# Kernel tuning notes

Hardware: AMD Instinct MI355X
Metric: run time of the kernel (lower is better)

Reference implementation:

```python
import jax, jax.numpy as jnp
import numpy as np

DIM = 512        # model dim
MOE_DIM = 256    # expert hidden dim
E = 64           # n_routed experts
G = 8            # n_routed_group
TOPK_G = 4       # n_topk_group
K = 8            # n_experts_per_tok
SCALE = 2.5      # routed_scale
CAP = 1024


def setup_inputs() -> dict:
    key = jax.random.key(0)
    ks = jax.random.split(key, 6)
    x = jax.random.normal(ks[0], (4, 512, DIM), jnp.float32)
    gate_w = jax.random.normal(ks[1], (E, DIM), jnp.float32) / np.sqrt(DIM).astype(np.float32)
    gate_b = jax.random.normal(ks[2], (E,), jnp.float32) * 0.01
    w1 = jax.random.normal(ks[3], (E, DIM, MOE_DIM), jnp.float32) / np.sqrt(DIM).astype(np.float32)
    w3 = jax.random.normal(ks[4], (E, DIM, MOE_DIM), jnp.float32) / np.sqrt(DIM).astype(np.float32)
    w2 = jax.random.normal(ks[5], (E, MOE_DIM, DIM), jnp.float32) / np.sqrt(MOE_DIM).astype(np.float32)
    return {"x": x, "gate_w": gate_w, "gate_b": gate_b, "w1": w1, "w3": w3, "w2": w2}


def _gate(x2, gate_w, gate_b):
    # x2: [T, DIM] -> (weights [T,K], indices [T,K])
    T = x2.shape[0]
    scores = jax.nn.sigmoid(x2 @ gate_w.T)                      # [T, E]
    s = (scores + gate_b).reshape(T, G, E // G)                  # grouped scores
    group_scores = jax.lax.top_k(s, 2)[0].sum(-1)                # [T, G] sum of top-2 per group
    top_groups = jax.lax.top_k(group_scores, TOPK_G)[1]          # [T, TOPK_G]
    gmask = jnp.zeros((T, G), bool).at[jnp.arange(T)[:, None], top_groups].set(True)
    s = jnp.where(gmask[..., None], s, -jnp.inf).reshape(T, E)
    idx = jax.lax.top_k(s, K)[1]                                 # [T, K]
    w = jnp.take_along_axis(scores, idx, axis=1)                 # original (pre-bias) scores
    w = w / w.sum(-1, keepdims=True) * SCALE
    return w, idx


def _moe_forward(x, gate_w, gate_b, w1, w3, w2):
    shape = x.shape
    x2 = x.reshape(-1, DIM)                                      # [T, DIM]
    T = x2.shape[0]
    w, idx = _gate(x2, gate_w, gate_b)
    flat_e = idx.reshape(-1)                                     # [T*K]
    # position of each (token, slot) within its expert's buffer, in order
    oh = (flat_e[:, None] == jnp.arange(E)[None, :]).astype(jnp.int32)  # [T*K, E]
    pos = (jnp.cumsum(oh, axis=0) * oh).sum(-1) - 1              # [T*K]
    x_rep = jnp.repeat(x2, K, axis=0)                            # [T*K, DIM]
    # dispatch into per-expert buffers [E, CAP, DIM]
    xb = jnp.zeros((E, CAP, DIM), x2.dtype).at[flat_e, pos].set(x_rep, mode='drop')
    h = jax.nn.silu(jnp.einsum('ecd,edm->ecm', xb, w1)) * jnp.einsum('ecd,edm->ecm', xb, w3)
    yb = jnp.einsum('ecm,emd->ecd', h, w2)                       # [E, CAP, DIM]
    # combine: gather back and weight
    y = yb.at[flat_e, pos].get(mode='fill', fill_value=0.0) * w.reshape(-1)[:, None]
    return y.reshape(T, K, DIM).sum(1).reshape(shape)


def reference(x, gate_w, gate_b, w1, w3, w2):
    return _moe_forward(x, gate_w, gate_b, w1, w3, w2)
```

## Files before the change

kernel.cpp:

```cpp
#include <hip/hip_runtime.h>

#define T_TOK 2048
#define DIM   512
#define MOE   256
#define NE    64
#define NG    8
#define TOPKG 4
#define TOPK  8
#define CAP   1024
#define MOE_SCALE 2.5f

typedef float f32x4 __attribute__((ext_vector_type(4)));
typedef short s16x8 __attribute__((ext_vector_type(8)));

__device__ __forceinline__ unsigned short f2bf(float f) {
    unsigned u = __builtin_bit_cast(unsigned, f);
    unsigned r = (u + 0x7fffu + ((u >> 16) & 1u)) >> 16;
    return (unsigned short)r;
}
__device__ __forceinline__ unsigned pk2(float lo, float hi) {
    return (unsigned)f2bf(lo) | ((unsigned)f2bf(hi) << 16);
}

__device__ __forceinline__ void tile_scan(const int* __restrict__ counts, int lane,
                                          int e, int& G0, int& ne, int& nt)
{
    int cl = min(counts[lane], CAP);
    int ntl = (cl + 31) >> 5;
    int v = ntl;
#pragma unroll
    for (int d = 1; d < 64; d <<= 1) {
        int o = __shfl_up(v, d);
        if (lane >= d) v += o;
    }
    G0 = __shfl(v - ntl, e);
    ne = __shfl(cl, e);
    nt = __shfl(ntl, e);
}

__global__ __launch_bounds__(256) void gwt_k(const float* __restrict__ gw,
                                             float* __restrict__ gwT)
{
    int idx = blockIdx.x * 256 + threadIdx.x;
    int e = idx >> 9, k = idx & 511;
    gwT[(size_t)(k >> 2) * 256 + e * 4 + (k & 3)] = gw[idx];
}

__global__ __launch_bounds__(256) void gate_fused_k(const float* __restrict__ x,
                                                    const float* __restrict__ gwT,
                                                    const float* __restrict__ gb,
                                                    int* __restrict__ counts,
                                                    int* __restrict__ etok,
                                                    float* __restrict__ wt_of,
                                                    short* __restrict__ xb)
{
    __shared__ float xs[4][512];
    __shared__ float ps[4][4][64];
    int w = threadIdx.x >> 6, lane = threadIdx.x & 63;
    int t = blockIdx.x * 4 + w;

    {
        const float4* xr = (const float4*)(x + (size_t)t * DIM);
        float4 v0 = xr[lane * 2], v1 = xr[lane * 2 + 1];
        *(float4*)&xs[w][lane * 8]     = v0;
        *(float4*)&xs[w][lane * 8 + 4] = v1;
        short o[8];
        o[0] = (short)f2bf(v0.x); o[1] = (short)f2bf(v0.y);
        o[2] = (short)f2bf(v0.z); o[3] = (short)f2bf(v0.w);
        o[4] = (short)f2bf(v1.x); o[5] = (short)f2bf(v1.y);
        o[6] = (short)f2bf(v1.z); o[7] = (short)f2bf(v1.w);
        *(s16x8*)(xb + (size_t)t * DIM + lane * 8) = *(const s16x8*)o;
    }
    __syncthreads();

    const f32x4* gt = (const f32x4*)gwT;
    float a0 = 0.f, a1 = 0.f, a2 = 0.f, a3 = 0.f;
    int kb = w * 32;
#pragma unroll 8
    for (int k4 = 0; k4 < 32; ++k4) {
        f32x4 g  = gt[(size_t)(kb + k4) * 64 + lane];
        f32x4 x0 = *(const f32x4*)&xs[0][(kb + k4) * 4];
        f32x4 x1 = *(const f32x4*)&xs[1][(kb + k4) * 4];
        f32x4 x2 = *(const f32x4*)&xs[2][(kb + k4) * 4];
        f32x4 x3 = *(const f32x4*)&xs[3][(kb + k4) * 4];
        a0 += g.x * x0.x + g.y * x0.y + g.z * x0.z + g.w * x0.w;
        a1 += g.x * x1.x + g.y * x1.y + g.z * x1.z + g.w * x1.w;
        a2 += g.x * x2.x + g.y * x2.y + g.z * x2.z + g.w * x2.w;
        a3 += g.x * x3.x + g.y * x3.y + g.z * x3.z + g.w * x3.w;
    }
    ps[w][0][lane] = a0; ps[w][1][lane] = a1;
    ps[w][2][lane] = a2; ps[w][3][lane] = a3;
    __syncthreads();
    float acc = ps[0][w][lane] + ps[1][w][lane] + ps[2][w][lane] + ps[3][w][lane];

    float sc = 1.f / (1.f + __expf(-acc));
    float s  = sc + gb[lane];

    float m1 = s, m2 = -1e30f;
#pragma unroll
    for (int d = 1; d < 8; d <<= 1) {
        float o1 = __shfl_xor(m1, d);
        float o2 = __shfl_xor(m2, d);
        float n1 = fmaxf(m1, o1);
        float n2 = fmaxf(fminf(m1, o1), fmaxf(m2, o2));
        m1 = n1; m2 = n2;
    }
    float gv = m1 + m2;

    bool gkeep = false;
#pragma unroll
    for (int it = 0; it < TOPKG; ++it) {
        float m = gv;
#pragma unroll
        for (int d = 1; d < 64; d <<= 1) m = fmaxf(m, __shfl_xor(m, d));
        unsigned long long mask = __ballot(gv == m);
        int ldr = __ffsll(mask) - 1;
        if ((lane >> 3) == (ldr >> 3)) { gkeep = true; gv = -2e30f; }
    }
    float sv = gkeep ? s : -1e30f;

    float wsum = 0.f;
    int my_e = 0; float my_w = 0.f;
#pragma unroll
    for (int k = 0; k < TOPK; ++k) {
        float m = sv;
#pragma unroll
        for (int d = 1; d < 64; d <<= 1) m = fmaxf(m, __shfl_xor(m, d));
        unsigned long long mask = __ballot(sv == m);
        int l = __ffsll(mask) - 1;
        float wk = __shfl(sc, l);
        wsum += wk;
        if (lane == k) { my_e = l; my_w = wk; }
        if (lane == l) sv = -2e30f;
    }
    float scale = MOE_SCALE / wsum;
    if (lane < TOPK) {
        int p = atomicAdd(&counts[my_e], 1);
        int rid = t * TOPK + lane;
        bool ok = (p < CAP);
        if (ok) etok[my_e * CAP + p] = rid;
        wt_of[rid] = ok ? my_w * scale : 0.f;
    }
}

__global__ __launch_bounds__(256, 2) void gemm1_k(const short* __restrict__ xb,
                                                  const float* __restrict__ w1,
                                                  const float* __restrict__ w3,
                                                  const int* __restrict__ counts,
                                                  const int* __restrict__ etok,
                                                  short* __restrict__ hgf)
{
    __shared__ short Bl[2][16][2][64][8];
    __shared__ short Ct[4][2][16][24];

    int e  = blockIdx.x & 63, cg = blockIdx.x >> 6;
    int n0 = cg * 32;
    int tid = threadIdx.x;
    int w = tid >> 6, lane = tid & 63;
    int q = lane >> 4, m16 = lane & 15;

    int G0, ne, nt;
    tile_scan(counts, lane, e, G0, ne, nt);

    const float* W1e = w1 + (size_t)e * DIM * MOE + n0;
    const float* W3e = w3 + (size_t)e * DIM * MOE + n0;
#pragma unroll 4
    for (int it = 0; it < 16; ++it) {
        int idx = it * 256 + tid;
        int mat = idx >> 11;
        int rem = idx & 2047;
        int r2  = rem >> 3;
        int cq  = (rem & 7) * 4;
        int k   = r2 * 2;
        int kt = k >> 5, qf = (k >> 3) & 3, j0 = k & 7;
        int cgrp = cq >> 4, c15 = cq & 15;
        const float* p = (mat ? W3e : W1e) + (size_t)k * MOE + cq;
        f32x4 lo = *(const f32x4*)p;
        f32x4 hi = *(const f32x4*)(p + MOE);
        unsigned* b = (unsigned*)&Bl[mat][kt][cgrp][qf * 16 + c15][j0];
        b[0]  = pk2(lo.x, hi.x);
        b[4]  = pk2(lo.y, hi.y);
        b[8]  = pk2(lo.z, hi.z);
        b[12] = pk2(lo.w, hi.w);
    }
    __syncthreads();

    const int* el = etok + e * CAP;

    int row0 = w * 32 + m16, row1 = row0 + 16;
    int tr0 = 0, tr1 = 0;
    if (w < nt) {
        tr0 = el[row0 < ne ? row0 : ne - 1];
        tr1 = el[row1 < ne ? row1 : ne - 1];
    }

    for (int T = w; T < nt; T += 4) {
        const short* A0 = xb + (size_t)(tr0 >> 3) * DIM + q * 8;
        const short* A1 = xb + (size_t)(tr1 >> 3) * DIM + q * 8;
        if (T + 4 < nt) {
            int nr0 = (T + 4) * 32 + m16, nr1 = nr0 + 16;
            tr0 = el[nr0 < ne ? nr0 : ne - 1];
            tr1 = el[nr1 < ne ? nr1 : ne - 1];
        }

        f32x4 acc[2][2][2];
#pragma unroll
        for (int i = 0; i < 2; ++i)
#pragma unroll
            for (int j = 0; j < 2; ++j)
#pragma unroll
                for (int c = 0; c < 2; ++c) acc[i][j][c] = (f32x4)0.f;

        s16x8 pa0[8], pa1[8];
#pragma unroll
        for (int i = 0; i < 8; ++i) {
            pa0[i] = *(const s16x8*)(A0 + i * 32);
            pa1[i] = *(const s16x8*)(A1 + i * 32);
        }
#pragma unroll
        for (int kt = 0; kt < 16; ++kt) {
            s16x8 a0 = pa0[kt & 7], a1 = pa1[kt & 7];
            if (kt < 8) {
                pa0[kt & 7] = *(const s16x8*)(A0 + (kt + 8) * 32);
                pa1[kt & 7] = *(const s16x8*)(A1 + (kt + 8) * 32);
            }
            s16x8 b10 = *(const s16x8*)&Bl[0][kt][0][lane][0];
            s16x8 b11 = *(const s16x8*)&Bl[0][kt][1][lane][0];
            s16x8 b30 = *(const s16x8*)&Bl[1][kt][0][lane][0];
            s16x8 b31 = *(const s16x8*)&Bl[1][kt][1][lane][0];
            acc[0][0][0] = __builtin_amdgcn_mfma_f32_16x16x32_bf16(a0, b10, acc[0][0][0], 0, 0, 0);
            acc[1][0][0] = __builtin_amdgcn_mfma_f32_16x16x32_bf16(a1, b10, acc[1][0][0], 0, 0, 0);
            acc[0][0][1] = __builtin_amdgcn_mfma_f32_16x16x32_bf16(a0, b11, acc[0][0][1], 0, 0, 0);
            acc[1][0][1] = __builtin_amdgcn_mfma_f32_16x16x32_bf16(a1, b11, acc[1][0][1], 0, 0, 0);
            acc[0][1][0] = __builtin_amdgcn_mfma_f32_16x16x32_bf16(a0, b30, acc[0][1][0], 0, 0, 0);
            acc[1][1][0] = __builtin_amdgcn_mfma_f32_16x16x32_bf16(a1, b30, acc[1][1][0], 0, 0, 0);
            acc[0][1][1] = __builtin_amdgcn_mfma_f32_16x16x32_bf16(a0, b31, acc[0][1][1], 0, 0, 0);
            acc[1][1][1] = __builtin_amdgcn_mfma_f32_16x16x32_bf16(a1, b31, acc[1][1][1], 0, 0, 0);
        }

#pragma unroll
        for (int cgrp = 0; cgrp < 2; ++cgrp) {
#pragma unroll
            for (int sub = 0; sub < 2; ++sub)
#pragma unroll
                for (int r = 0; r < 4; ++r) {
                    float g = acc[sub][0][cgrp][r];
                    float u = acc[sub][1][cgrp][r];
                    float hv = g / (1.f + __expf(-g)) * u;
                    Ct[w][sub][q * 4 + r][m16] = (short)f2bf(hv);
                }
            int subr = q >> 1;
            s16x8 hv8 = *(const s16x8*)&Ct[w][subr][m16][(q & 1) * 8];
            size_t slot = ((size_t)(G0 + T) * 8 + cg) * 2 + subr;
            *(s16x8*)(hgf + slot * 512 + (cgrp * 2 + (q & 1)) * 128 + m16 * 8) = hv8;
        }
    }
}

__global__ __launch_bounds__(256, 2) void gemm2_k(const short* __restrict__ hgf,
                                                  const float* __restrict__ w2,
                                                  const int* __restrict__ counts,
                                                  const int* __restrict__ etok,
                                                  const float* __restrict__ wt_of,
                                                  float* __restrict__ out)
{
    __shared__ short Bl[4][8][64][8];

    int e  = blockIdx.x & 63, cg = blockIdx.x >> 6;
    int n0 = cg * 64;
    int tid = threadIdx.x;
    int w = tid >> 6, lane = tid & 63;
    int q = lane >> 4, m16 = lane & 15;

    int G0, ne, nt;
    tile_scan(counts, lane, e, G0, ne, nt);

    const float* W2e = w2 + (size_t)e * MOE * DIM + n0;
#pragma unroll 4
    for (int it = 0; it < 8; ++it) {
        int idx = it * 256 + tid;
        int r2  = idx >> 4;
        int cq  = (idx & 15) * 4;
        int k   = r2 * 2;
        int kt2 = k >> 5, qf = (k >> 3) & 3, j0 = k & 7;
        int s = cq >> 4, c15 = cq & 15;
        const float* p = W2e + (size_t)k * DIM + cq;
        f32x4 lo = *(const f32x4*)p;
        f32x4 hi = *(const f32x4*)(p + DIM);
        unsigned* b = (unsigned*)&Bl[s][kt2][qf * 16 + c15][j0];
        b[0]  = pk2(lo.x, hi.x);
        b[4]  = pk2(lo.y, hi.y);
        b[8]  = pk2(lo.z, hi.z);
        b[12] = pk2(lo.w, hi.w);
    }
    __syncthreads();

    const int* el = etok + e * CAP;

    for (int T = w; T < nt; T += 4) {
        const short* A = hgf + (size_t)(G0 + T) * 8192 + lane * 8;

        int   erid[2][4];
        float wtr[2][4];
#pragma unroll
        for (int sub = 0; sub < 2; ++sub)
#pragma unroll
            for (int r = 0; r < 4; ++r) {
                int row = T * 32 + sub * 16 + q * 4 + r;
                int rid = row < ne ? el[row] : -1;
                erid[sub][r] = rid;
                wtr[sub][r]  = rid >= 0 ? wt_of[rid] : 0.f;
            }

        s16x8 pa[16];
#pragma unroll
        for (int i = 0; i < 16; ++i)
            pa[i] = *(const s16x8*)(A + i * 512);

        f32x4 acc[2][4];
#pragma unroll
        for (int i = 0; i < 2; ++i)
#pragma unroll
            for (int j = 0; j < 4; ++j) acc[i][j] = (f32x4)0.f;

#pragma unroll
        for (int kt = 0; kt < 8; ++kt) {
            s16x8 a0 = pa[kt * 2], a1 = pa[kt * 2 + 1];
            s16x8 b0 = *(const s16x8*)&Bl[0][kt][lane][0];
            s16x8 b1 = *(const s16x8*)&Bl[1][kt][lane][0];
            s16x8 b2 = *(const s16x8*)&Bl[2][kt][lane][0];
            s16x8 b3 = *(const s16x8*)&Bl[3][kt][lane][0];
            acc[0][0] = __builtin_amdgcn_mfma_f32_16x16x32_bf16(a0, b0, acc[0][0], 0, 0, 0);
            acc[1][0] = __builtin_amdgcn_mfma_f32_16x16x32_bf16(a1, b0, acc[1][0], 0, 0, 0);
            acc[0][1] = __builtin_amdgcn_mfma_f32_16x16x32_bf16(a0, b1, acc[0][1], 0, 0, 0);
            acc[1][1] = __builtin_amdgcn_mfma_f32_16x16x32_bf16(a1, b1, acc[1][1], 0, 0, 0);
            acc[0][2] = __builtin_amdgcn_mfma_f32_16x16x32_bf16(a0, b2, acc[0][2], 0, 0, 0);
            acc[1][2] = __builtin_amdgcn_mfma_f32_16x16x32_bf16(a1, b2, acc[1][2], 0, 0, 0);
            acc[0][3] = __builtin_amdgcn_mfma_f32_16x16x32_bf16(a0, b3, acc[0][3], 0, 0, 0);
            acc[1][3] = __builtin_amdgcn_mfma_f32_16x16x32_bf16(a1, b3, acc[1][3], 0, 0, 0);
        }

#pragma unroll
        for (int sub = 0; sub < 2; ++sub)
#pragma unroll
            for (int r = 0; r < 4; ++r) {
                int rid = erid[sub][r];
                if (rid >= 0) {
                    float* op = out + (size_t)(rid >> 3) * DIM + n0 + m16;
                    float wk = wtr[sub][r];
#pragma unroll
                    for (int s = 0; s < 4; ++s)
                        atomicAdd(op + s * 16, wk * acc[sub][s][r]);
                }
            }
    }
}

extern "C" void kernel_launch(void* const* d_in, const int* in_sizes, int n_in,
                              void* d_out, int out_size, void* d_ws, size_t ws_size,
                              hipStream_t stream)
{
    const float* x  = (const float*)d_in[0];
    const float* gw = (const float*)d_in[1];
    const float* gb = (const float*)d_in[2];
    const float* w1 = (const float*)d_in[3];
    const float* w3 = (const float*)d_in[4];
    const float* w2 = (const float*)d_in[5];

    char* ws = (char*)d_ws;
    short* xb    = (short*)(ws);
    short* hgf   = (short*)(ws + 2097152);
    float* gwT   = (float*)(ws + 28311552);
    int*   etok  = (int*)  (ws + 28442624);
    float* wt_of = (float*)(ws + 28704768);
    int*   counts= (int*)  (ws + 28770304);

    hipMemsetAsync(counts, 0, NE * 4, stream);
    hipMemsetAsync(d_out, 0, (size_t)T_TOK * DIM * 4, stream);

    gwt_k<<<128, 256, 0, stream>>>(gw, gwT);
    gate_fused_k<<<T_TOK / 4, 256, 0, stream>>>(x, gwT, gb, counts, etok, wt_of, xb);
    gemm1_k<<<NE * 8, 256, 0, stream>>>(xb, w1, w3, counts, etok, hgf);
    gemm2_k<<<NE * 8, 256, 0, stream>>>(hgf, w2, counts, etok, wt_of, (float*)d_out);
}
```

Measured before the change: 270.1 us.

## Replace atomic scatter-add with bf16 per-slot buffer and combine kernel; double block size

gemm2 now writes each expert output row as bf16 into a per-(token,slot) buffer instead of doing fp32 atomicAdd into the output. A new combine kernel then sums the 8 weighted slots per token, which also removes the output memset. Both GEMM kernels move to 512-thread blocks with 8 waves sharing the staged weight tile, and the weight loads become nontemporal. The trade is an extra kernel launch, a round trip through a buffer, and bf16 rounding of the expert outputs before they are combined.

```diff
diff --git a/kernel.cpp b/kernel.cpp
--- a/kernel.cpp
+++ b/kernel.cpp
@@ -143,7 +143,7 @@
     }
 }
 
-__global__ __launch_bounds__(256, 2) void gemm1_k(const short* __restrict__ xb,
+__global__ __launch_bounds__(512, 4) void gemm1_k(const short* __restrict__ xb,
                                                   const float* __restrict__ w1,
                                                   const float* __restrict__ w3,
                                                   const int* __restrict__ counts,
@@ -151,7 +151,7 @@
                                                   short* __restrict__ hgf)
 {
     __shared__ short Bl[2][16][2][64][8];
-    __shared__ short Ct[4][2][16][24];
+    __shared__ short Ct[8][2][16][24];
 
     int e  = blockIdx.x & 63, cg = blockIdx.x >> 6;
     int n0 = cg * 32;
@@ -165,8 +165,8 @@
     const float* W1e = w1 + (size_t)e * DIM * MOE + n0;
     const float* W3e = w3 + (size_t)e * DIM * MOE + n0;
 #pragma unroll 4
-    for (int it = 0; it < 16; ++it) {
-        int idx = it * 256 + tid;
+    for (int it = 0; it < 8; ++it) {
+        int idx = it * 512 + tid;
         int mat = idx >> 11;
         int rem = idx & 2047;
         int r2  = rem >> 3;
@@ -175,8 +175,8 @@
         int kt = k >> 5, qf = (k >> 3) & 3, j0 = k & 7;
         int cgrp = cq >> 4, c15 = cq & 15;
         const float* p = (mat ? W3e : W1e) + (size_t)k * MOE + cq;
-        f32x4 lo = *(const f32x4*)p;
-        f32x4 hi = *(const f32x4*)(p + MOE);
+        f32x4 lo = __builtin_nontemporal_load((const f32x4*)p);
+        f32x4 hi = __builtin_nontemporal_load((const f32x4*)(p + MOE));
         unsigned* b = (unsigned*)&Bl[mat][kt][cgrp][qf * 16 + c15][j0];
         b[0]  = pk2(lo.x, hi.x);
         b[4]  = pk2(lo.y, hi.y);
@@ -194,11 +194,11 @@
         tr1 = el[row1 < ne ? row1 : ne - 1];
     }
 
-    for (int T = w; T < nt; T += 4) {
+    for (int T = w; T < nt; T += 8) {
         const short* A0 = xb + (size_t)(tr0 >> 3) * DIM + q * 8;
         const short* A1 = xb + (size_t)(tr1 >> 3) * DIM + q * 8;
-        if (T + 4 < nt) {
-            int nr0 = (T + 4) * 32 + m16, nr1 = nr0 + 16;
+        if (T + 8 < nt) {
+            int nr0 = (T + 8) * 32 + m16, nr1 = nr0 + 16;
             tr0 = el[nr0 < ne ? nr0 : ne - 1];
             tr1 = el[nr1 < ne ? nr1 : ne - 1];
         }
@@ -257,12 +257,11 @@
     }
 }
 
-__global__ __launch_bounds__(256, 2) void gemm2_k(const short* __restrict__ hgf,
+__global__ __launch_bounds__(512, 4) void gemm2_k(const short* __restrict__ hgf,
                                                   const float* __restrict__ w2,
                                                   const int* __restrict__ counts,
                                                   const int* __restrict__ etok,
-                                                  const float* __restrict__ wt_of,
-                                                  float* __restrict__ out)
+                                                  short* __restrict__ ybuf)
 {
     __shared__ short Bl[4][8][64][8];
 
@@ -277,16 +276,16 @@
 
     const float* W2e = w2 + (size_t)e * MOE * DIM + n0;
 #pragma unroll 4
-    for (int it = 0; it < 8; ++it) {
-        int idx = it * 256 + tid;
+    for (int it = 0; it < 4; ++it) {
+        int idx = it * 512 + tid;
         int r2  = idx >> 4;
         int cq  = (idx & 15) * 4;
         int k   = r2 * 2;
         int kt2 = k >> 5, qf = (k >> 3) & 3, j0 = k & 7;
         int s = cq >> 4, c15 = cq & 15;
         const float* p = W2e + (size_t)k * DIM + cq;
-        f32x4 lo = *(const f32x4*)p;
-        f32x4 hi = *(const f32x4*)(p + DIM);
+        f32x4 lo = __builtin_nontemporal_load((const f32x4*)p);
+        f32x4 hi = __builtin_nontemporal_load((const f32x4*)(p + DIM));
         unsigned* b = (unsigned*)&Bl[s][kt2][qf * 16 + c15][j0];
         b[0]  = pk2(lo.x, hi.x);
         b[4]  = pk2(lo.y, hi.y);
@@ -297,19 +296,16 @@
 
     const int* el = etok + e * CAP;
 
-    for (int T = w; T < nt; T += 4) {
+    for (int T = w; T < nt; T += 8) {
         const short* A = hgf + (size_t)(G0 + T) * 8192 + lane * 8;
 
-        int   erid[2][4];
-        float wtr[2][4];
+        int erid[2][4];
 #pragma unroll
         for (int sub = 0; sub < 2; ++sub)
 #pragma unroll
             for (int r = 0; r < 4; ++r) {
                 int row = T * 32 + sub * 16 + q * 4 + r;
-                int rid = row < ne ? el[row] : -1;
-                erid[sub][r] = rid;
-                wtr[sub][r]  = rid >= 0 ? wt_of[rid] : 0.f;
+                erid[sub][r] = row < ne ? el[row] : -1;
             }
 
         s16x8 pa[16];
@@ -343,17 +339,35 @@
 #pragma unroll
         for (int sub = 0; sub < 2; ++sub)
 #pragma unroll
-            for (int r = 0; r < 4; ++r) {
-                int rid = erid[sub][r];
-                if (rid >= 0) {
-                    float* op = out + (size_t)(rid >> 3) * DIM + n0 + m16;
-                    float wk = wtr[sub][r];
-#pragma unroll
-                    for (int s = 0; s < 4; ++s)
-                        atomicAdd(op + s * 16, wk * acc[sub][s][r]);
+            for (int s = 0; s < 4; ++s)
+#pragma unroll
+                for (int r = 0; r < 4; ++r) {
+                    if (erid[sub][r] >= 0)
+                        ybuf[(size_t)erid[sub][r] * DIM + n0 + s * 16 + m16] =
+                            (short)f2bf(acc[sub][s][r]);
                 }
-            }
-    }
+    }
+}
+
+__global__ __launch_bounds__(256) void combine_k(const short* __restrict__ ybuf,
+                                                 const float* __restrict__ wt_of,
+                                                 float* __restrict__ out)
+{
+    int t = blockIdx.x;
+    int tid = threadIdx.x;
+    const int* yb = (const int*)ybuf;
+    float sx = 0.f, sy = 0.f;
+#pragma unroll
+    for (int k = 0; k < TOPK; ++k) {
+        float wk = wt_of[t * TOPK + k];
+        int v = yb[(size_t)(t * TOPK + k) * (DIM / 2) + tid];
+        float lo = __builtin_bit_cast(float, (unsigned)v << 16);
+        float hi = __builtin_bit_cast(float, (unsigned)v & 0xffff0000u);
+        sx += wk * lo;
+        sy += wk * hi;
+    }
+    float2 o = {sx, sy};
+    ((float2*)out)[(size_t)t * (DIM / 2) + tid] = o;
 }
 
 extern "C" void kernel_launch(void* const* d_in, const int* in_sizes, int n_in,
@@ -370,16 +384,17 @@
     char* ws = (char*)d_ws;
     short* xb    = (short*)(ws);
     short* hgf   = (short*)(ws + 2097152);
+    short* ybuf  = (short*)(ws + 11534336);
     float* gwT   = (float*)(ws + 28311552);
     int*   etok  = (int*)  (ws + 28442624);
     float* wt_of = (float*)(ws + 28704768);
     int*   counts= (int*)  (ws + 28770304);
 
     hipMemsetAsync(counts, 0, NE * 4, stream);
-    hipMemsetAsync(d_out, 0, (size_t)T_TOK * DIM * 4, stream);
 
     gwt_k<<<128, 256, 0, stream>>>(gw, gwT);
     gate_fused_k<<<T_TOK / 4, 256, 0, stream>>>(x, gwT, gb, counts, etok, wt_of, xb);
-    gemm1_k<<<NE * 8, 256, 0, stream>>>(xb, w1, w3, counts, etok, hgf);
-    gemm2_k<<<NE * 8, 256, 0, stream>>>(hgf, w2, counts, etok, wt_of, (float*)d_out);
-}
+    gemm1_k<<<NE * 8, 512, 0, stream>>>(xb, w1, w3, counts, etok, hgf);
+    gemm2_k<<<NE * 8, 512, 0, stream>>>(hgf, w2, counts, etok, ybuf);
+    combine_k<<<T_TOK, 256, 0, stream>>>(ybuf, wt_of, (float*)d_out);
+}
```

After: 302.0 us. +11.8%, slower.
